# Performance work log

Hardware: AMD Instinct MI355X
Metric: run time of the kernel (lower is better)

## Reference

```python
import jax, jax.numpy as jnp
import numpy as np


def setup_inputs() -> dict:
    key = jax.random.key(0)
    k1, k2 = jax.random.split(key)
    x = jax.random.normal(k1, (4, 11, 64, 96, 96), dtype=jnp.float32)
    gamma = jax.random.normal(k2, (1,), dtype=jnp.float32) * 0.1
    return {"x": x, "gamma": gamma}


def reference(x, gamma):
    # x: (B, N, C, H, W)
    B, N, C, H, W = x.shape
    q = x.reshape(B, N, C * H * W)  # (B, N, D)

    # Gram matrix: energy2[b,i,j] = <q_i, q_j>
    energy2 = jnp.einsum('bnd,bmd->bnm', q, q)  # (B, N, N)

    # Pairwise L1 distance energy1[b,i,j] = sum_d |q_i - q_j|.
    # Loop over small fixed N=11 rows to avoid a (B,N,N,D) intermediate.
    rows = [jnp.sum(jnp.abs(q - q[:, i:i + 1, :]), axis=-1) for i in range(N)]
    energy1 = jnp.stack(rows, axis=1)  # (B, N, N)
    # Original torch writes into energy1.data -> no gradient flows through it.
    energy1 = jax.lax.stop_gradient(energy1)

    energy = energy1 * energy2
    energy_new = jnp.max(energy, axis=-1, keepdims=True) - energy
    attention = jax.nn.softmax(energy_new, axis=-1)  # (B, N, N)

    out = jnp.einsum('bnm,bmd->bnd', attention, q)  # (B, N, D)
    out = out.reshape(B, N, C, H, W)
    out = gamma * out + x
    return out.reshape(B, N * C, H, W)
```

## Files before the change

### kernel.cpp

```cpp
#include <hip/hip_runtime.h>

#define B_    4
#define N_    11
#define D_    589824L
#define NPAIR 66
#define TPB   256
#define ITER  8

__global__ __launch_bounds__(TPB) void reduce_kernel(const float* __restrict__ x,
                                                     double* __restrict__ e2ws,
                                                     double* __restrict__ e1ws) {
    const int b = blockIdx.y;
    const int t = threadIdx.x;
    const long base = (long)blockIdx.x * (TPB * 4 * ITER) + (long)t * 4;
    const float* xb = x + (long)b * N_ * D_;

    float acc2[NPAIR];
    float acc1[NPAIR];
#pragma unroll
    for (int p = 0; p < NPAIR; ++p) { acc2[p] = 0.f; acc1[p] = 0.f; }

#pragma unroll 1
    for (int k = 0; k < ITER; ++k) {
        const long d = base + (long)k * (TPB * 4);
        float4 v[N_];
#pragma unroll
        for (int m = 0; m < N_; ++m)
            v[m] = *reinterpret_cast<const float4*>(xb + (long)m * D_ + d);

        int p = 0;
#pragma unroll
        for (int i = 0; i < N_; ++i) {
#pragma unroll
            for (int j = i; j < N_; ++j) {
                acc2[p] += v[i].x * v[j].x + v[i].y * v[j].y +
                           v[i].z * v[j].z + v[i].w * v[j].w;
                if (i != j) {
                    acc1[p] += fabsf(v[i].x - v[j].x) + fabsf(v[i].y - v[j].y) +
                               fabsf(v[i].z - v[j].z) + fabsf(v[i].w - v[j].w);
                }
                ++p;
            }
        }
    }

    __shared__ float red2[TPB / 64][NPAIR];
    __shared__ float red1[TPB / 64][NPAIR];
    const int wave = t >> 6, lane = t & 63;
#pragma unroll
    for (int p = 0; p < NPAIR; ++p) {
        float s2 = acc2[p], s1 = acc1[p];
#pragma unroll
        for (int off = 32; off > 0; off >>= 1) {
            s2 += __shfl_down(s2, off, 64);
            s1 += __shfl_down(s1, off, 64);
        }
        if (lane == 0) { red2[wave][p] = s2; red1[wave][p] = s1; }
    }
    __syncthreads();
    if (t < NPAIR) {
        float s2 = 0.f, s1 = 0.f;
#pragma unroll
        for (int w = 0; w < TPB / 64; ++w) { s2 += red2[w][t]; s1 += red1[w][t]; }
        atomicAdd(&e2ws[b * NPAIR + t], (double)s2);
        atomicAdd(&e1ws[b * NPAIR + t], (double)s1);
    }
}

__global__ __launch_bounds__(128) void attn_kernel(const double* __restrict__ e2ws,
                                                   const double* __restrict__ e1ws,
                                                   const float* __restrict__ gamma,
                                                   float* __restrict__ Mws) {
    const int b = blockIdx.x;
    const int t = threadIdx.x;
    __shared__ double E[N_][N_];
    if (t < NPAIR) {
        int rem = t, i = 0, cnt = N_;
        while (rem >= cnt) { rem -= cnt; --cnt; ++i; }
        const int j = i + rem;
        const double e = e1ws[b * NPAIR + t] * e2ws[b * NPAIR + t];
        E[i][j] = e;
        E[j][i] = e;
    }
    __syncthreads();
    if (t < N_) {
        const int i = t;
        double mn = E[i][0];
#pragma unroll
        for (int j = 1; j < N_; ++j) mn = fmin(mn, E[i][j]);
        double ex[N_], s = 0.0;
#pragma unroll
        for (int j = 0; j < N_; ++j) { ex[j] = exp(mn - E[i][j]); s += ex[j]; }
        const float g = gamma[0];
        const double inv = 1.0 / s;
#pragma unroll
        for (int j = 0; j < N_; ++j) {
            float m = (float)(ex[j] * inv) * g + (i == j ? 1.0f : 0.0f);
            Mws[(b * N_ + i) * N_ + j] = m;
        }
    }
}

__global__ __launch_bounds__(TPB) void apply_kernel(const float* __restrict__ x,
                                                    const float* __restrict__ Mws,
                                                    float* __restrict__ out) {
    const int b = blockIdx.y;
    const int t = threadIdx.x;
    __shared__ float M[N_ * N_];
    if (t < N_ * N_) M[t] = Mws[b * N_ * N_ + t];
    __syncthreads();

    const long d = (long)blockIdx.x * (TPB * 4) + (long)t * 4;
    const float* xb = x + (long)b * N_ * D_;
    float* ob = out + (long)b * N_ * D_;

    float4 v[N_];
#pragma unroll
    for (int m = 0; m < N_; ++m)
        v[m] = *reinterpret_cast<const float4*>(xb + (long)m * D_ + d);

#pragma unroll
    for (int n = 0; n < N_; ++n) {
        float4 o = make_float4(0.f, 0.f, 0.f, 0.f);
#pragma unroll
        for (int m = 0; m < N_; ++m) {
            const float w = M[n * N_ + m];
            o.x += w * v[m].x;
            o.y += w * v[m].y;
            o.z += w * v[m].z;
            o.w += w * v[m].w;
        }
        *reinterpret_cast<float4*>(ob + (long)n * D_ + d) = o;
    }
}

extern "C" void kernel_launch(void* const* d_in, const int* in_sizes, int n_in,
                              void* d_out, int out_size, void* d_ws, size_t ws_size,
                              hipStream_t stream) {
    const float* x     = (const float*)d_in[0];
    const float* gamma = (const float*)d_in[1];
    float* out         = (float*)d_out;

    double* e2ws = (double*)d_ws;
    double* e1ws = e2ws + B_ * NPAIR;
    float*  Mws  = (float*)(e1ws + B_ * NPAIR);

    hipMemsetAsync(d_ws, 0, (size_t)(2 * B_ * NPAIR) * sizeof(double), stream);

    dim3 gridA(D_ / (TPB * 4 * ITER), B_);
    reduce_kernel<<<gridA, TPB, 0, stream>>>(x, e2ws, e1ws);

    attn_kernel<<<B_, 128, 0, stream>>>(e2ws, e1ws, gamma, Mws);

    dim3 gridC(D_ / (TPB * 4), B_);
    apply_kernel<<<gridC, TPB, 0, stream>>>(x, Mws, out);
}
```

Before: 267.7 us.

## Split pair reduction into three chunks across grid z to cut register pressure

The 66 pair accumulators are split into three chunks of 22. Each chunk gets its own template instantiation, selected by blockIdx.z, and loads only the rows its pairs use. Fewer accumulators per thread lower register use, and together with launch_bounds(TPB,4) and ITER halved to 4 this should raise occupancy and the number of blocks in flight. The cost is that x is read up to three times, since each chunk still loads most of the 11 rows, and there are more atomics.

```diff
diff --git a/kernel.cpp b/kernel.cpp
--- a/kernel.cpp
+++ b/kernel.cpp
@@ -1,24 +1,39 @@
 #include <hip/hip_runtime.h>
 
-#define B_    4
-#define N_    11
-#define D_    589824L
-#define NPAIR 66
-#define TPB   256
-#define ITER  8
+#define B_     4
+#define N_     11
+#define D_     589824L
+#define NPAIR  66
+#define NCHUNK 3
+#define CP     22
+#define TPB    256
+#define ITER   4
 
-__global__ __launch_bounds__(TPB) void reduce_kernel(const float* __restrict__ x,
-                                                     double* __restrict__ e2ws,
-                                                     double* __restrict__ e1ws) {
-    const int b = blockIdx.y;
-    const int t = threadIdx.x;
-    const long base = (long)blockIdx.x * (TPB * 4 * ITER) + (long)t * 4;
-    const float* xb = x + (long)b * N_ * D_;
+__host__ __device__ constexpr int pair_i(int p) {
+    int i = 0, cnt = N_;
+    while (p >= cnt) { p -= cnt; --cnt; ++i; }
+    return i;
+}
+__host__ __device__ constexpr int pair_j(int p) {
+    int i = 0, cnt = N_;
+    while (p >= cnt) { p -= cnt; --cnt; ++i; }
+    return i + p;
+}
+__host__ __device__ constexpr bool row_used(int chunk, int m) {
+    for (int q = 0; q < CP; ++q) {
+        const int p = chunk * CP + q;
+        if (pair_i(p) == m || pair_j(p) == m) return true;
+    }
+    return false;
+}
 
-    float acc2[NPAIR];
-    float acc1[NPAIR];
+template <int CHUNK>
+__device__ void reduce_body(const float* __restrict__ xb, long base, int b, int t,
+                            double* __restrict__ e2ws, double* __restrict__ e1ws) {
+    float acc2[CP];
+    float acc1[CP];
 #pragma unroll
-    for (int p = 0; p < NPAIR; ++p) { acc2[p] = 0.f; acc1[p] = 0.f; }
+    for (int q = 0; q < CP; ++q) { acc2[q] = 0.f; acc1[q] = 0.f; }
 
 #pragma unroll 1
     for (int k = 0; k < ITER; ++k) {
@@ -26,44 +41,56 @@
         float4 v[N_];
 #pragma unroll
         for (int m = 0; m < N_; ++m)
-            v[m] = *reinterpret_cast<const float4*>(xb + (long)m * D_ + d);
+            if (row_used(CHUNK, m))
+                v[m] = *reinterpret_cast<const float4*>(xb + (long)m * D_ + d);
 
-        int p = 0;
 #pragma unroll
-        for (int i = 0; i < N_; ++i) {
-#pragma unroll
-            for (int j = i; j < N_; ++j) {
-                acc2[p] += v[i].x * v[j].x + v[i].y * v[j].y +
-                           v[i].z * v[j].z + v[i].w * v[j].w;
-                if (i != j) {
-                    acc1[p] += fabsf(v[i].x - v[j].x) + fabsf(v[i].y - v[j].y) +
-                               fabsf(v[i].z - v[j].z) + fabsf(v[i].w - v[j].w);
-                }
-                ++p;
+        for (int q = 0; q < CP; ++q) {
+            const int i = pair_i(CHUNK * CP + q);
+            const int j = pair_j(CHUNK * CP + q);
+            acc2[q] += v[i].x * v[j].x + v[i].y * v[j].y +
+                       v[i].z * v[j].z + v[i].w * v[j].w;
+            if (i != j) {
+                acc1[q] += fabsf(v[i].x - v[j].x) + fabsf(v[i].y - v[j].y) +
+                           fabsf(v[i].z - v[j].z) + fabsf(v[i].w - v[j].w);
             }
         }
     }
 
-    __shared__ float red2[TPB / 64][NPAIR];
-    __shared__ float red1[TPB / 64][NPAIR];
+    __shared__ float red2[TPB / 64][CP];
+    __shared__ float red1[TPB / 64][CP];
     const int wave = t >> 6, lane = t & 63;
 #pragma unroll
-    for (int p = 0; p < NPAIR; ++p) {
-        float s2 = acc2[p], s1 = acc1[p];
+    for (int q = 0; q < CP; ++q) {
+        float s2 = acc2[q], s1 = acc1[q];
 #pragma unroll
         for (int off = 32; off > 0; off >>= 1) {
             s2 += __shfl_down(s2, off, 64);
             s1 += __shfl_down(s1, off, 64);
         }
-        if (lane == 0) { red2[wave][p] = s2; red1[wave][p] = s1; }
+        if (lane == 0) { red2[wave][q] = s2; red1[wave][q] = s1; }
     }
     __syncthreads();
-    if (t < NPAIR) {
+    if (t < CP) {
         float s2 = 0.f, s1 = 0.f;
 #pragma unroll
         for (int w = 0; w < TPB / 64; ++w) { s2 += red2[w][t]; s1 += red1[w][t]; }
-        atomicAdd(&e2ws[b * NPAIR + t], (double)s2);
-        atomicAdd(&e1ws[b * NPAIR + t], (double)s1);
+        atomicAdd(&e2ws[b * NPAIR + CHUNK * CP + t], (double)s2);
+        atomicAdd(&e1ws[b * NPAIR + CHUNK * CP + t], (double)s1);
+    }
+}
+
+__global__ __launch_bounds__(TPB, 4) void reduce_kernel(const float* __restrict__ x,
+                                                        double* __restrict__ e2ws,
+                                                        double* __restrict__ e1ws) {
+    const int b = blockIdx.y;
+    const int t = threadIdx.x;
+    const long base = (long)blockIdx.x * (TPB * 4 * ITER) + (long)t * 4;
+    const float* xb = x + (long)b * N_ * D_;
+    switch (blockIdx.z) {
+        case 0:  reduce_body<0>(xb, base, b, t, e2ws, e1ws); break;
+        case 1:  reduce_body<1>(xb, base, b, t, e2ws, e1ws); break;
+        default: reduce_body<2>(xb, base, b, t, e2ws, e1ws); break;
     }
 }
 
@@ -147,7 +174,7 @@
 
     hipMemsetAsync(d_ws, 0, (size_t)(2 * B_ * NPAIR) * sizeof(double), stream);
 
-    dim3 gridA(D_ / (TPB * 4 * ITER), B_);
+    dim3 gridA(D_ / (TPB * 4 * ITER), B_, NCHUNK);
     reduce_kernel<<<gridA, TPB, 0, stream>>>(x, e2ws, e1ws);
 
     attn_kernel<<<B_, 128, 0, stream>>>(e2ws, e1ws, gamma, Mws);
```

Result: slower. 629.4 us (+135.1%).
